# Kernel optimization log

Hardware: AMD Instinct MI355X
Metric: run time of the kernel (lower is better)

Reference implementation:

```python
import jax, jax.numpy as jnp
import numpy as np

B, D_MODEL, H, W = 4, 128, 128, 128
HEAD_DIM = 16
GROUP = D_MODEL // HEAD_DIM          # 8 deformable groups
D_INNER = D_MODEL                    # expand = 1
D_STATE = 1
DT_RANK = 8                          # ceil(d_model / 16)
D_CONV = 3
EPS = 1e-6


def setup_inputs() -> dict:
    key = jax.random.key(0)
    ks = jax.random.split(key, 10)
    f = jnp.float32
    # dt bias init as in DASSM.dt_init (dt in [1e-3, 1e-1], inverse-softplus)
    dt = jnp.exp(jax.random.uniform(ks[7], (D_INNER,), f)
                 * (np.log(0.1) - np.log(0.001)) + np.log(0.001))
    dt = jnp.clip(dt, 1e-4)
    dt_b = dt + jnp.log(-jnp.expm1(-dt))
    s = DT_RANK ** -0.5
    return dict(
        x=jax.random.normal(ks[0], (B, D_MODEL, H, W), f),
        in_proj_w=jax.random.normal(ks[1], (D_INNER, D_MODEL), f) * (D_MODEL ** -0.5),
        conv2d_w=jax.random.normal(ks[2], (D_INNER, 1, D_CONV, D_CONV), f) * 0.1,
        conv2d_b=jnp.zeros((D_INNER,), f),
        dw_w=jax.random.normal(ks[3], (D_INNER, 1, 3, 3), f) * 0.1,
        dw_b=jnp.zeros((D_INNER,), f),
        dw_ln_g=jnp.ones((D_INNER,), f),
        dw_ln_b=jnp.zeros((D_INNER,), f),
        off_w=jax.random.normal(ks[4], (GROUP * 2, D_INNER), f) * 0.01,
        off_b=jnp.zeros((GROUP * 2,), f),
        x_proj_w=jax.random.normal(ks[5], (DT_RANK + 2 * D_STATE, D_INNER), f) * (D_INNER ** -0.5),
        dt_w=jax.random.uniform(ks[6], (D_INNER, DT_RANK), f, -s, s),
        dt_b=dt_b,
        A_logs=jnp.tile(jnp.log(jnp.arange(1, D_STATE + 1, dtype=f))[None, :], (D_INNER, 1)),
        Ds=jnp.ones((D_INNER,), f),
        out_ln_g=jnp.ones((D_INNER,), f),
        out_ln_b=jnp.zeros((D_INNER,), f),
        out_proj_w=jax.random.normal(ks[8], (D_MODEL, D_INNER), f) * (D_INNER ** -0.5),
    )


def _layer_norm(x, g, b):
    m = x.mean(-1, keepdims=True)
    v = ((x - m) ** 2).mean(-1, keepdims=True)
    return (x - m) * jax.lax.rsqrt(v + EPS) * g + b


def _dwconv(x, w, b):
    # x: (B,C,H,W), w: (C,1,k,k) depthwise, 'SAME' == torch padding=(k-1)//2
    out = jax.lax.conv_general_dilated(
        x, w, (1, 1), 'SAME', feature_group_count=x.shape[1],
        dimension_numbers=('NCHW', 'OIHW', 'NCHW'))
    return out + b[None, :, None, None]


def _dcn_sample(img_last, offset):
    # DCNv3 with kernel_size=1, mask=1: sampling point = pixel center + offset.
    # img_last: (B,H,W,C); offset: (B,H,W,G*2) laid out (x,y) per group.
    b, h, w, c = img_last.shape
    gc = c // GROUP
    img = img_last.reshape(b, h, w, GROUP, gc)
    off = offset.reshape(b, h, w, GROUP, 2)
    px = jnp.arange(w, dtype=offset.dtype)[None, None, :, None] + off[..., 0]
    py = jnp.arange(h, dtype=offset.dtype)[None, :, None, None] + off[..., 1]
    y0 = jnp.floor(py)
    x0 = jnp.floor(px)
    wy = py - y0
    wx = px - x0
    bi = jnp.arange(b)[:, None, None, None]
    gi = jnp.arange(GROUP)[None, None, None, :]

    def tap(yi, xi, wgt):  # zero-padding bilinear tap (grid_sample, align_corners=False)
        valid = (yi >= 0) & (yi < h) & (xi >= 0) & (xi < w)
        yc = jnp.clip(yi, 0, h - 1).astype(jnp.int32)
        xc = jnp.clip(xi, 0, w - 1).astype(jnp.int32)
        v = img[bi, yc, xc, gi]  # (B,H,W,G,gc)
        return v * (wgt * valid)[..., None]

    out = (tap(y0, x0, (1 - wy) * (1 - wx)) + tap(y0, x0 + 1, (1 - wy) * wx)
           + tap(y0 + 1, x0, wy * (1 - wx)) + tap(y0 + 1, x0 + 1, wy * wx))
    return out.reshape(b, h, w, c)


def _selective_scan(xs, dts, A, Bs, Cs, Ds, dt_bias):
    # xs,dts: (B,D,L); A: (D,N); Bs,Cs: (B,N,L); delta_softplus=True
    delta = jax.nn.softplus(dts + dt_bias[None, :, None])
    dA = jnp.exp(jnp.einsum('bdl,dn->lbdn', delta, A))          # (L,B,D,N)
    dBx = jnp.einsum('bdl,bnl,bdl->lbdn', delta, Bs, xs)          # (L,B,D,N)
    C_t = jnp.transpose(Cs, (2, 0, 1))                            # (L,B,N)

    def step(hc, inputs):
        dA_t, dBx_t, c = inputs
        hc = dA_t * hc + dBx_t
        return hc, jnp.einsum('bdn,bn->bd', hc, c)

    h0 = jnp.zeros(dA.shape[1:], xs.dtype)
    _, ys = jax.lax.scan(step, h0, (dA, dBx, C_t))                # ys: (L,B,D)
    y = jnp.transpose(ys, (1, 2, 0))                              # (B,D,L)
    return y + Ds[None, :, None] * xs


def reference(x, in_proj_w, conv2d_w, conv2d_b, dw_w, dw_b, dw_ln_g, dw_ln_b,
              off_w, off_b, x_proj_w, dt_w, dt_b, A_logs, Ds,
              out_ln_g, out_ln_b, out_proj_w):
    # in_proj (1x1 conv, no bias) then depthwise conv + SiLU
    xin = jnp.einsum('bchw,oc->bohw', x, in_proj_w)
    xc = jax.nn.silu(_dwconv(xin, conv2d_w, conv2d_b))
    # Dynamic_Adaptive_Scan: dwconv -> LN(channels_last) -> GELU -> offsets -> DCNv3(k=1)
    x1 = _dwconv(xc, dw_w, dw_b)
    x1 = jax.nn.gelu(_layer_norm(jnp.transpose(x1, (0, 2, 3, 1)), dw_ln_g, dw_ln_b),
                     approximate=False)
    offset = x1 @ off_w.T + off_b                                  # (B,H,W,G*2)
    xd = _dcn_sample(jnp.transpose(xc, (0, 2, 3, 1)), offset)      # (B,H,W,C)
    xd = jnp.transpose(xd, (0, 3, 1, 2))                           # (B,C,H,W)
    # SSM (Mamba selective scan over L = H*W)
    Bn, C, Hh, Ww = xd.shape
    L = Hh * Ww
    xs = xd.reshape(Bn, C, L)
    x_dbl = jnp.einsum('rc,bcl->brl', x_proj_w, xs)
    dts, Bs, Cs = jnp.split(x_dbl, [DT_RANK, DT_RANK + D_STATE], axis=1)
    dts = jnp.einsum('dr,brl->bdl', dt_w, dts)
    A = -jnp.exp(A_logs)
    y = _selective_scan(xs, dts, A, Bs, Cs, Ds, dt_b).reshape(Bn, C, Hh, Ww)
    # out LayerNorm (over channels) + out_proj (1x1, no bias)
    y = jnp.transpose(_layer_norm(jnp.transpose(y, (0, 2, 3, 1)), out_ln_g, out_ln_b),
                      (0, 3, 1, 2))
    return jnp.einsum('bchw,oc->bohw', y, out_proj_w)
```

## Files before the change

kernel.cpp:

```cpp
#include <hip/hip_runtime.h>
#include <hip/hip_bf16.h>

typedef unsigned short u16;
typedef unsigned int u32;
typedef __bf16 bf16x8 __attribute__((ext_vector_type(8)));
typedef float f32x4 __attribute__((ext_vector_type(4)));

__device__ __forceinline__ float bfu(u16 u) { return __uint_as_float(((u32)u) << 16); }
__device__ __forceinline__ u16 fbf(float f) {
  __hip_bfloat16 h = __float2bfloat16(f);
  return *reinterpret_cast<u16*>(&h);
}
__device__ __forceinline__ float softplusf(float z) {
  float t = __expf(z);
  return (z > 20.f) ? z : __logf(1.f + t);
}
__device__ __forceinline__ float lo16(u32 p) { return __uint_as_float(p << 16); }
__device__ __forceinline__ float hi16(u32 p) { return __uint_as_float(p & 0xffff0000u); }
__device__ __forceinline__ bf16x8 ld_bf8(const u16* p) {
  union { uint4 u; bf16x8 v; } c;
  c.u = *(const uint4*)p;
  return c.v;
}

__global__ __launch_bounds__(256) void k_inproj(const float* __restrict__ X,
                                                const float* __restrict__ W,
                                                u16* __restrict__ out) {
  __shared__ __align__(16) u16 Ws[128 * 136];
  __shared__ __align__(16) u16 Xs[64 * 136];
  int tid = threadIdx.x;
  int b = blockIdx.x >> 8;
  int l0 = (blockIdx.x & 255) << 6;
  for (int i = 0; i < 16; ++i) {
    int idx = (i << 8) + tid;
    int o = idx >> 5, c4 = (idx & 31) << 2;
    float4 w4 = *(const float4*)&W[(o << 7) + c4];
    ushort4 s;
    s.x = fbf(w4.x); s.y = fbf(w4.y); s.z = fbf(w4.z); s.w = fbf(w4.w);
    *(ushort4*)&Ws[o * 136 + c4] = s;
  }
  for (int i = 0; i < 8; ++i) {
    int idx = (i << 8) + tid;
    int c = idx >> 4, lq = (idx & 15) << 2;
    float4 x4 = *(const float4*)&X[(((long)(b << 7) + c) << 14) + l0 + lq];
    Xs[(lq + 0) * 136 + c] = fbf(x4.x);
    Xs[(lq + 1) * 136 + c] = fbf(x4.y);
    Xs[(lq + 2) * 136 + c] = fbf(x4.z);
    Xs[(lq + 3) * 136 + c] = fbf(x4.w);
  }
  __syncthreads();
  int w = tid >> 6, lane = tid & 63;
  int mrow = lane & 15, quad = lane >> 4;
  f32x4 acc[2][4];
#pragma unroll
  for (int ot = 0; ot < 2; ++ot)
#pragma unroll
    for (int lt = 0; lt < 4; ++lt) acc[ot][lt] = (f32x4){0.f, 0.f, 0.f, 0.f};
#pragma unroll
  for (int kb = 0; kb < 4; ++kb) {
    int c0 = (kb << 5) + (quad << 3);
    bf16x8 af[2], bfr[4];
#pragma unroll
    for (int ot = 0; ot < 2; ++ot)
      af[ot] = ld_bf8(&Ws[((w << 5) + (ot << 4) + mrow) * 136 + c0]);
#pragma unroll
    for (int lt = 0; lt < 4; ++lt)
      bfr[lt] = ld_bf8(&Xs[((lt << 4) + mrow) * 136 + c0]);
#pragma unroll
    for (int ot = 0; ot < 2; ++ot)
#pragma unroll
      for (int lt = 0; lt < 4; ++lt)
        acc[ot][lt] = __builtin_amdgcn_mfma_f32_16x16x32_bf16(af[ot], bfr[lt], acc[ot][lt], 0, 0, 0);
  }
#pragma unroll
  for (int ot = 0; ot < 2; ++ot)
#pragma unroll
    for (int lt = 0; lt < 4; ++lt) {
      int l = l0 + (lt << 4) + mrow;
      int o = (w << 5) + (ot << 4) + (quad << 2);
      ushort4 s;
      s.x = fbf(acc[ot][lt][0]); s.y = fbf(acc[ot][lt][1]);
      s.z = fbf(acc[ot][lt][2]); s.w = fbf(acc[ot][lt][3]);
      *(ushort4*)&out[(((long)(b << 14) + l) << 7) + o] = s;
    }
}

__global__ __launch_bounds__(256) void k_dwconv(const u16* __restrict__ in,
                                                const float* __restrict__ w9,
                                                const float* __restrict__ bias,
                                                u16* __restrict__ out, int act) {
  __shared__ float wsT[9][128];
  __shared__ float bs[128];
  int tid = threadIdx.x;
  for (int i = 0; i < 5; ++i) {
    int lin = (i << 8) + tid;
    if (lin < 1152) { int c = lin / 9, k = lin - 9 * c; wsT[k][c] = w9[lin]; }
  }
  if (tid < 128) bs[tid] = bias[tid];
  __syncthreads();
  int blk = blockIdx.x;
  int b = blk >> 10;
  int s = blk & 1023;
  int h = s >> 3;
  int w = ((s & 7) << 4) + (tid >> 4);
  int c0 = (tid & 15) << 3;
  const u16* bbase = in + ((long)b << 21);
  float acc[8];
  {
    float4 b0 = *(const float4*)&bs[c0];
    float4 b1 = *(const float4*)&bs[c0 + 4];
    acc[0] = b0.x; acc[1] = b0.y; acc[2] = b0.z; acc[3] = b0.w;
    acc[4] = b1.x; acc[5] = b1.y; acc[6] = b1.z; acc[7] = b1.w;
  }
#pragma unroll
  for (int ky = -1; ky <= 1; ++ky) {
    int y = h + ky;
    if ((unsigned)y >= 128u) continue;
#pragma unroll
    for (int kx = -1; kx <= 1; ++kx) {
      int x = w + kx;
      if ((unsigned)x >= 128u) continue;
      int k = (ky + 1) * 3 + (kx + 1);
      uint4 v = *(const uint4*)(bbase + ((((y << 7) + x)) << 7) + c0);
      float4 w0 = *(const float4*)&wsT[k][c0];
      float4 w1 = *(const float4*)&wsT[k][c0 + 4];
      u32 vv[4] = {v.x, v.y, v.z, v.w};
      float wf[8] = {w0.x, w0.y, w0.z, w0.w, w1.x, w1.y, w1.z, w1.w};
#pragma unroll
      for (int cc = 0; cc < 8; ++cc) {
        float xv = (cc & 1) ? hi16(vv[cc >> 1]) : lo16(vv[cc >> 1]);
        acc[cc] = fmaf(wf[cc], xv, acc[cc]);
      }
    }
  }
  if (act) {
#pragma unroll
    for (int cc = 0; cc < 8; ++cc) acc[cc] = acc[cc] / (1.f + __expf(-acc[cc]));
  }
  ushort4 s0, s1;
  s0.x = fbf(acc[0]); s0.y = fbf(acc[1]); s0.z = fbf(acc[2]); s0.w = fbf(acc[3]);
  s1.x = fbf(acc[4]); s1.y = fbf(acc[5]); s1.z = fbf(acc[6]); s1.w = fbf(acc[7]);
  u16* po = out + ((long)b << 21) + ((((h << 7) + w)) << 7) + c0;
  *(ushort4*)po = s0;
  *(ushort4*)(po + 4) = s1;
}

__global__ __launch_bounds__(256) void k_offset(const u16* __restrict__ x1,
                                                const float* __restrict__ g,
                                                const float* __restrict__ bt,
                                                const float* __restrict__ offw,
                                                const float* __restrict__ offb,
                                                float* __restrict__ offs) {
  __shared__ float Wo[16 * 128];
  __shared__ float gs[128], bsh[128];
  int tid = threadIdx.x;
  if (tid < 128) { gs[tid] = g[tid]; bsh[tid] = bt[tid]; }
  for (int i = 0; i < 8; ++i) { int idx = (i << 8) + tid; Wo[idx] = offw[idx]; }
  __syncthreads();
  int pg = (blockIdx.x << 8) + tid;
  int b = pg >> 14, l = pg & 16383;
  const uint4* px = (const uint4*)(x1 + ((long)pg << 7));
  float s = 0.f, ss = 0.f;
  for (int i = 0; i < 16; ++i) {
    uint4 v = px[i];
    u32 vv[4] = {v.x, v.y, v.z, v.w};
#pragma unroll
    for (int cc = 0; cc < 8; ++cc) {
      float xv = (cc & 1) ? hi16(vv[cc >> 1]) : lo16(vv[cc >> 1]);
      s += xv; ss = fmaf(xv, xv, ss);
    }
  }
  float mean = s * (1.f / 128.f);
  float var = ss * (1.f / 128.f) - mean * mean;
  float rstd = rsqrtf(var + 1e-6f);
  float acc[16];
#pragma unroll
  for (int j = 0; j < 16; ++j) acc[j] = offb[j];
  for (int i = 0; i < 16; ++i) {
    uint4 v = px[i];
    u32 vv[4] = {v.x, v.y, v.z, v.w};
#pragma unroll
    for (int cc = 0; cc < 8; ++cc) {
      int c = (i << 3) + cc;
      float xv = (cc & 1) ? hi16(vv[cc >> 1]) : lo16(vv[cc >> 1]);
      float xn = fmaf((xv - mean) * rstd, gs[c], bsh[c]);
      float ge = 0.5f * xn * (1.f + erff(xn * 0.70710678118f));
#pragma unroll
      for (int j = 0; j < 16; ++j) acc[j] = fmaf(Wo[j * 128 + c], ge, acc[j]);
    }
  }
  float2* po = (float2*)offs;
#pragma unroll
  for (int gg = 0; gg < 8; ++gg)
    po[(((long)((b << 3) + gg)) << 14) + l] = make_float2(acc[2 * gg], acc[2 * gg + 1]);
}

__global__ __launch_bounds__(256) void k_dcn(const u16* __restrict__ xc,
                                             const float* __restrict__ offs,
                                             const float* __restrict__ xpw,
                                             const float* __restrict__ dtw,
                                             u16* __restrict__ xs,
                                             u16* __restrict__ dts,
                                             float* __restrict__ Bsb,
                                             float* __restrict__ Csb) {
  __shared__ float xds[32 * 129];
  __shared__ float xdbl[32 * 13];
  __shared__ float xpws[1280];
  __shared__ float dtws[1024];
  int tid = threadIdx.x;
  for (int i = 0; i < 5; ++i) { int idx = (i << 8) + tid; if (idx < 1280) xpws[idx] = xpw[idx]; }
  for (int i = 0; i < 4; ++i) { int idx = (i << 8) + tid; dtws[idx] = dtw[idx]; }
  int blk = blockIdx.x;
  int b = blk >> 9;
  int l0 = (blk & 511) << 5;
  int p = tid & 31, gg = tid >> 5;
  int l = l0 + p, hh = l >> 7, ww = l & 127;
  float2 off = ((const float2*)offs)[(((long)((b << 3) + gg)) << 14) + l];
  float px = (float)ww + off.x, py = (float)hh + off.y;
  float x0f = floorf(px), y0f = floorf(py);
  float wx = px - x0f, wy = py - y0f;
  int ix = (int)x0f, iy = (int)y0f;
  float acc[16];
#pragma unroll
  for (int ch = 0; ch < 16; ++ch) acc[ch] = 0.f;
  const u16* bbase = xc + ((long)b << 21) + (gg << 4);
  int xi[4] = {ix, ix + 1, ix, ix + 1};
  int yi[4] = {iy, iy, iy + 1, iy + 1};
  float wt4[4] = {(1.f - wy) * (1.f - wx), (1.f - wy) * wx, wy * (1.f - wx), wy * wx};
#pragma unroll
  for (int t = 0; t < 4; ++t) {
    if (wt4[t] != 0.f && (unsigned)yi[t] < 128u && (unsigned)xi[t] < 128u) {
      const u16* pp = bbase + ((((yi[t] << 7) + xi[t])) << 7);
      uint4 v0 = *(const uint4*)pp;
      uint4 v1 = *(const uint4*)(pp + 8);
      float wv = wt4[t];
      u32 vv[8] = {v0.x, v0.y, v0.z, v0.w, v1.x, v1.y, v1.z, v1.w};
#pragma unroll
      for (int ch = 0; ch < 16; ++ch) {
        float xv = (ch & 1) ? hi16(vv[ch >> 1]) : lo16(vv[ch >> 1]);
        acc[ch] = fmaf(wv, xv, acc[ch]);
      }
    }
  }
#pragma unroll
  for (int ch = 0; ch < 16; ++ch) xds[p * 129 + (gg << 4) + ch] = acc[ch];
  __syncthreads();
  for (int it = 0; it < 4; ++it) {
    int task = (it << 8) + tid;
    int cc = task >> 3, t = task & 7;
    ushort4 s;
    s.x = fbf(xds[(4 * t + 0) * 129 + cc]);
    s.y = fbf(xds[(4 * t + 1) * 129 + cc]);
    s.z = fbf(xds[(4 * t + 2) * 129 + cc]);
    s.w = fbf(xds[(4 * t + 3) * 129 + cc]);
    *(ushort4*)&xs[(((long)(b << 7) + cc) << 14) + l0 + (t << 2)] = s;
  }
  for (int task = tid; task < 320; task += 256) {
    int p2 = task / 10, r = task - p2 * 10;
    const float* wr = xpws + (r << 7);
    const float* xr = xds + p2 * 129;
    float sacc = 0.f;
#pragma unroll 8
    for (int cc = 0; cc < 128; ++cc) sacc = fmaf(wr[cc], xr[cc], sacc);
    xdbl[p2 * 13 + r] = sacc;
  }
  __syncthreads();
  for (int it = 0; it < 4; ++it) {
    int task = (it << 8) + tid;
    int dd = task >> 3, t = task & 7;
    const float* wd = dtws + (dd << 3);
    u16 sv[4];
#pragma unroll
    for (int j = 0; j < 4; ++j) {
      const float* xb = xdbl + (4 * t + j) * 13;
      float sacc = 0.f;
#pragma unroll
      for (int r = 0; r < 8; ++r) sacc = fmaf(wd[r], xb[r], sacc);
      sv[j] = fbf(sacc);
    }
    ushort4 s; s.x = sv[0]; s.y = sv[1]; s.z = sv[2]; s.w = sv[3];
    *(ushort4*)&dts[(((long)(b << 7) + dd) << 14) + l0 + (t << 2)] = s;
  }
  if (tid < 32) {
    Bsb[((long)b << 14) + l0 + tid] = xdbl[tid * 13 + 8];
    Csb[((long)b << 14) + l0 + tid] = xdbl[tid * 13 + 9];
  }
}

__global__ __launch_bounds__(1024) void k_scan(u16* __restrict__ xy,
                                               const u16* __restrict__ dts16,
                                               const float* __restrict__ Bsb,
                                               const float* __restrict__ Csb,
                                               const float* __restrict__ A_logs,
                                               const float* __restrict__ Dsv,
                                               const float* __restrict__ dtbv) {
  __shared__ float swp[16], swe[16];
  int bd = blockIdx.x;
  int b = bd >> 7, d = bd & 127;
  float Ad = -__expf(A_logs[d]);
  float dtb = dtbv[d];
  float Dd = Dsv[d];
  int t = threadIdx.x;
  int lane = t & 63, wid = t >> 6;
  long base = ((long)bd << 14) + (t << 4);
  long bb = ((long)b << 14) + (t << 4);
  const uint4* pz4 = (const uint4*)(dts16 + base);
  const uint4* px4 = (const uint4*)(xy + base);
  const float4* pB = (const float4*)(Bsb + bb);
  const float4* pC = (const float4*)(Csb + bb);
  uint4 zA = pz4[0], zB = pz4[1];
  uint4 xA = px4[0], xB = px4[1];
  u32 zw[8] = {zA.x, zA.y, zA.z, zA.w, zB.x, zB.y, zB.z, zB.w};
  u32 xw[8] = {xA.x, xA.y, xA.z, xA.w, xB.x, xB.y, xB.z, xB.w};
  float E = 0.f, P = 1.f;
#pragma unroll
  for (int q = 0; q < 4; ++q) {
    float4 B4 = pB[q];
    float Bq[4] = {B4.x, B4.y, B4.z, B4.w};
#pragma unroll
    for (int j = 0; j < 4; ++j) {
      int k = (q << 2) + j;
      float z = (k & 1) ? hi16(zw[k >> 1]) : lo16(zw[k >> 1]);
      float xv = (k & 1) ? hi16(xw[k >> 1]) : lo16(xw[k >> 1]);
      float delta = softplusf(z + dtb);
      float a = __expf(delta * Ad);
      E = fmaf(a, E, delta * Bq[j] * xv);
      P *= a;
    }
  }
#pragma unroll
  for (int off = 1; off < 64; off <<= 1) {
    float Pp = __shfl_up(P, off);
    float Ep = __shfl_up(E, off);
    if (lane >= off) { E = fmaf(P, Ep, E); P *= Pp; }
  }
  if (lane == 63) { swp[wid] = P; swe[wid] = E; }
  __syncthreads();
  if (t < 16) {
    float p2 = swp[t], e2 = swe[t];
#pragma unroll
    for (int off = 1; off < 16; off <<= 1) {
      float pp = __shfl_up(p2, off);
      float ee = __shfl_up(e2, off);
      if (t >= off) { e2 = fmaf(p2, ee, e2); p2 *= pp; }
    }
    swp[t] = p2; swe[t] = e2;
  }
  __syncthreads();
  float hw = (wid == 0) ? 0.f : swe[wid - 1];
  float Pex = __shfl_up(P, 1);
  float Eex = __shfl_up(E, 1);
  if (lane == 0) { Pex = 1.f; Eex = 0.f; }
  float h = fmaf(Pex, hw, Eex);
  u32 ypk[8];
#pragma unroll
  for (int q = 0; q < 4; ++q) {
    float4 B4 = pB[q];
    float4 C4 = pC[q];
    float Bq[4] = {B4.x, B4.y, B4.z, B4.w};
    float Cq[4] = {C4.x, C4.y, C4.z, C4.w};
#pragma unroll
    for (int j = 0; j < 4; ++j) {
      int k = (q << 2) + j;
      float z = (k & 1) ? hi16(zw[k >> 1]) : lo16(zw[k >> 1]);
      float xv = (k & 1) ? hi16(xw[k >> 1]) : lo16(xw[k >> 1]);
      float delta = softplusf(z + dtb);
      float a = __expf(delta * Ad);
      h = fmaf(a, h, delta * Bq[j] * xv);
      u16 yb = fbf(fmaf(Dd, xv, h * Cq[j]));
      if ((k & 1) == 0) ypk[k >> 1] = yb; else ypk[k >> 1] |= (u32)yb << 16;
    }
  }
  uint4* py = (uint4*)(xy + base);
  py[0] = make_uint4(ypk[0], ypk[1], ypk[2], ypk[3]);
  py[1] = make_uint4(ypk[4], ypk[5], ypk[6], ypk[7]);
}

__global__ void k_sums(const float* __restrict__ W2, const float* __restrict__ g,
                       const float* __restrict__ bln, float* __restrict__ s12) {
  int o = threadIdx.x;
  float s1 = 0.f, s2 = 0.f;
  for (int c = 0; c < 128; ++c) {
    float w = W2[(o << 7) + c];
    s1 = fmaf(w, bln[c], s1);
    s2 = fmaf(w, g[c], s2);
  }
  s12[o] = s1;
  s12[128 + o] = s2;
}

__global__ __launch_bounds__(256) void k_outproj(const u16* __restrict__ y,
                                                 const float* __restrict__ W2,
                                                 const float* __restrict__ g,
                                                 const float* __restrict__ s12,
                                                 float* __restrict__ out) {
  __shared__ __align__(16) u16 Ws[128 * 136];
  __shared__ __align__(16) u16 Ys[64 * 136];
  __shared__ float ps[4][64], pss[4][64];
  __shared__ float mean_s[64], rstd_s[64];
  int tid = threadIdx.x;
  int b = blockIdx.x >> 8;
  int l0 = (blockIdx.x & 255) << 6;
  for (int i = 0; i < 16; ++i) {
    int idx = (i << 8) + tid;
    int o = idx >> 5, c4 = (idx & 31) << 2;
    float4 w4 = *(const float4*)&W2[(o << 7) + c4];
    ushort4 s;
    s.x = fbf(w4.x * g[c4]);     s.y = fbf(w4.y * g[c4 + 1]);
    s.z = fbf(w4.z * g[c4 + 2]); s.w = fbf(w4.w * g[c4 + 3]);
    *(ushort4*)&Ws[o * 136 + c4] = s;
  }
  for (int i = 0; i < 4; ++i) {
    int idx = (i << 8) + tid;
    int c = idx >> 3, lq = (idx & 7) << 3;
    uint4 v = *(const uint4*)&y[(((long)(b << 7) + c) << 14) + l0 + lq];
    u32 vv[4] = {v.x, v.y, v.z, v.w};
#pragma unroll
    for (int r = 0; r < 8; ++r)
      Ys[(lq + r) * 136 + c] = (u16)((r & 1) ? (vv[r >> 1] >> 16) : (vv[r >> 1] & 0xffffu));
  }
  __syncthreads();
  {
    int l = tid & 63, q = tid >> 6;
    const u16* row = &Ys[l * 136 + (q << 5)];
    float s = 0.f, ss = 0.f;
#pragma unroll 8
    for (int c = 0; c < 32; ++c) { float v = bfu(row[c]); s += v; ss = fmaf(v, v, ss); }
    ps[q][l] = s; pss[q][l] = ss;
  }
  __syncthreads();
  if (tid < 64) {
    float s = ps[0][tid] + ps[1][tid] + ps[2][tid] + ps[3][tid];
    float ss = pss[0][tid] + pss[1][tid] + pss[2][tid] + pss[3][tid];
    float m = s * (1.f / 128.f);
    mean_s[tid] = m;
    rstd_s[tid] = rsqrtf(ss * (1.f / 128.f) - m * m + 1e-6f);
  }
  __syncthreads();
  int w = tid >> 6, lane = tid & 63;
  int mrow = lane & 15, quad = lane >> 4;
  f32x4 acc[2][4];
#pragma unroll
  for (int ot = 0; ot < 2; ++ot)
#pragma unroll
    for (int lt = 0; lt < 4; ++lt) acc[ot][lt] = (f32x4){0.f, 0.f, 0.f, 0.f};
#pragma unroll
  for (int kb = 0; kb < 4; ++kb) {
    int c0 = (kb << 5) + (quad << 3);
    bf16x8 af[2], bfr[4];
#pragma unroll
    for (int ot = 0; ot < 2; ++ot)
      af[ot] = ld_bf8(&Ws[((w << 5) + (ot << 4) + mrow) * 136 + c0]);
#pragma unroll
    for (int lt = 0; lt < 4; ++lt)
      bfr[lt] = ld_bf8(&Ys[((lt << 4) + mrow) * 136 + c0]);
#pragma unroll
    for (int ot = 0; ot < 2; ++ot)
#pragma unroll
      for (int lt = 0; lt < 4; ++lt)
        acc[ot][lt] = __builtin_amdgcn_mfma_f32_16x16x32_bf16(af[ot], bfr[lt], acc[ot][lt], 0, 0, 0);
  }
  float s1r[2][4], s2r[2][4];
#pragma unroll
  for (int ot = 0; ot < 2; ++ot)
#pragma unroll
    for (int r = 0; r < 4; ++r) {
      int o = (w << 5) + (ot << 4) + (quad << 2) + r;
      s1r[ot][r] = s12[o];
      s2r[ot][r] = s12[128 + o];
    }
#pragma unroll
  for (int ot = 0; ot < 2; ++ot)
#pragma unroll
    for (int lt = 0; lt < 4; ++lt) {
      int lcol = (lt << 4) + mrow;
      float mv = mean_s[lcol], rv = rstd_s[lcol];
      int obase = (w << 5) + (ot << 4) + (quad << 2);
#pragma unroll
      for (int r = 0; r < 4; ++r) {
        float v = fmaf(rv, acc[ot][lt][r] - mv * s2r[ot][r], s1r[ot][r]);
        out[(((long)(b << 7) + obase + r) << 14) + l0 + lcol] = v;
      }
    }
}

extern "C" void kernel_launch(void* const* d_in, const int* in_sizes, int n_in,
                              void* d_out, int out_size, void* d_ws, size_t ws_size,
                              hipStream_t stream) {
  const float* x         = (const float*)d_in[0];
  const float* in_proj_w = (const float*)d_in[1];
  const float* conv2d_w  = (const float*)d_in[2];
  const float* conv2d_b  = (const float*)d_in[3];
  const float* dw_w      = (const float*)d_in[4];
  const float* dw_b      = (const float*)d_in[5];
  const float* dw_ln_g   = (const float*)d_in[6];
  const float* dw_ln_b   = (const float*)d_in[7];
  const float* off_w     = (const float*)d_in[8];
  const float* off_b     = (const float*)d_in[9];
  const float* x_proj_w  = (const float*)d_in[10];
  const float* dt_w      = (const float*)d_in[11];
  const float* dt_b      = (const float*)d_in[12];
  const float* A_logs    = (const float*)d_in[13];
  const float* Ds        = (const float*)d_in[14];
  const float* out_ln_g  = (const float*)d_in[15];
  const float* out_ln_b  = (const float*)d_in[16];
  const float* out_proj_w= (const float*)d_in[17];
  float* out = (float*)d_out;

  u16* A  = (u16*)d_ws;
  u16* Bx = A + 8388608;
  u16* Dd = Bx + 8388608;
  float* offs  = (float*)(Dd + 8388608);
  float* Bsb   = offs + 1048576;
  float* Csb   = Bsb + 65536;
  float* s12   = Csb + 65536;

  hipLaunchKernelGGL(k_inproj, dim3(1024), dim3(256), 0, stream, x, in_proj_w, A);
  hipLaunchKernelGGL(k_dwconv, dim3(4096), dim3(256), 0, stream, A, conv2d_w, conv2d_b, Bx, 1);
  hipLaunchKernelGGL(k_dwconv, dim3(4096), dim3(256), 0, stream, Bx, dw_w, dw_b, A, 0);
  hipLaunchKernelGGL(k_offset, dim3(256), dim3(256), 0, stream, A, dw_ln_g, dw_ln_b, off_w, off_b, offs);
  hipLaunchKernelGGL(k_dcn, dim3(2048), dim3(256), 0, stream, Bx, offs, x_proj_w, dt_w, A, Dd, Bsb, Csb);
  hipLaunchKernelGGL(k_scan, dim3(512), dim3(1024), 0, stream, A, Dd, Bsb, Csb, A_logs, Ds, dt_b);
  hipLaunchKernelGGL(k_sums, dim3(1), dim3(128), 0, stream, out_proj_w, out_ln_g, out_ln_b, s12);
  hipLaunchKernelGGL(k_outproj, dim3(1024), dim3(256), 0, stream, A, out_proj_w, out_ln_g, s12, out);
}
```

Before: 246.7 us.

## Rewrite offset projection with MFMA and widen DCN tiles to 64 pixels

After: 235.7 us. -4.5%, faster.

```diff
diff --git a/kernel.cpp b/kernel.cpp
--- a/kernel.cpp
+++ b/kernel.cpp
@@ -151,51 +151,78 @@
                                                 const float* __restrict__ offw,
                                                 const float* __restrict__ offb,
                                                 float* __restrict__ offs) {
-  __shared__ float Wo[16 * 128];
+  __shared__ __align__(16) u16 Ge[64 * 136];
+  __shared__ __align__(16) u16 Wos[16 * 136];
+  __shared__ float ps[4][64], pss[4][64];
+  __shared__ float mean_s[64], rstd_s[64];
   __shared__ float gs[128], bsh[128];
   int tid = threadIdx.x;
+  int pg0 = blockIdx.x << 6;
+  int b = pg0 >> 14;
   if (tid < 128) { gs[tid] = g[tid]; bsh[tid] = bt[tid]; }
-  for (int i = 0; i < 8; ++i) { int idx = (i << 8) + tid; Wo[idx] = offw[idx]; }
-  __syncthreads();
-  int pg = (blockIdx.x << 8) + tid;
-  int b = pg >> 14, l = pg & 16383;
-  const uint4* px = (const uint4*)(x1 + ((long)pg << 7));
-  float s = 0.f, ss = 0.f;
-  for (int i = 0; i < 16; ++i) {
-    uint4 v = px[i];
-    u32 vv[4] = {v.x, v.y, v.z, v.w};
-#pragma unroll
-    for (int cc = 0; cc < 8; ++cc) {
-      float xv = (cc & 1) ? hi16(vv[cc >> 1]) : lo16(vv[cc >> 1]);
-      s += xv; ss = fmaf(xv, xv, ss);
-    }
-  }
-  float mean = s * (1.f / 128.f);
-  float var = ss * (1.f / 128.f) - mean * mean;
-  float rstd = rsqrtf(var + 1e-6f);
-  float acc[16];
-#pragma unroll
-  for (int j = 0; j < 16; ++j) acc[j] = offb[j];
-  for (int i = 0; i < 16; ++i) {
-    uint4 v = px[i];
-    u32 vv[4] = {v.x, v.y, v.z, v.w};
-#pragma unroll
-    for (int cc = 0; cc < 8; ++cc) {
-      int c = (i << 3) + cc;
-      float xv = (cc & 1) ? hi16(vv[cc >> 1]) : lo16(vv[cc >> 1]);
-      float xn = fmaf((xv - mean) * rstd, gs[c], bsh[c]);
-      float ge = 0.5f * xn * (1.f + erff(xn * 0.70710678118f));
-#pragma unroll
-      for (int j = 0; j < 16; ++j) acc[j] = fmaf(Wo[j * 128 + c], ge, acc[j]);
-    }
-  }
+  for (int i = 0; i < 8; ++i) {
+    int idx = (i << 8) + tid;
+    int o = idx >> 7, c = idx & 127;
+    Wos[o * 136 + c] = fbf(offw[idx]);
+  }
+  int l = tid >> 2, cq = (tid & 3) << 5;
+  {
+    const u16* px = x1 + (((long)(pg0 + l)) << 7) + cq;
+    float s = 0.f, ss = 0.f;
+#pragma unroll
+    for (int i2 = 0; i2 < 4; ++i2) {
+      uint4 v = *(const uint4*)(px + (i2 << 3));
+      *(uint4*)&Ge[l * 136 + cq + (i2 << 3)] = v;
+      u32 vv[4] = {v.x, v.y, v.z, v.w};
+#pragma unroll
+      for (int cc = 0; cc < 8; ++cc) {
+        float xv = (cc & 1) ? hi16(vv[cc >> 1]) : lo16(vv[cc >> 1]);
+        s += xv; ss = fmaf(xv, xv, ss);
+      }
+    }
+    ps[tid & 3][l] = s; pss[tid & 3][l] = ss;
+  }
+  __syncthreads();
+  if (tid < 64) {
+    float s = ps[0][tid] + ps[1][tid] + ps[2][tid] + ps[3][tid];
+    float ss = pss[0][tid] + pss[1][tid] + pss[2][tid] + pss[3][tid];
+    float m = s * (1.f / 128.f);
+    mean_s[tid] = m;
+    rstd_s[tid] = rsqrtf(ss * (1.f / 128.f) - m * m + 1e-6f);
+  }
+  __syncthreads();
+  {
+    float m = mean_s[l], r = rstd_s[l];
+    u16* row = &Ge[l * 136 + cq];
+#pragma unroll 8
+    for (int cc = 0; cc < 32; ++cc) {
+      int c = cq + cc;
+      float v = bfu(row[cc]);
+      float xn = fmaf((v - m) * r, gs[c], bsh[c]);
+      row[cc] = fbf(0.5f * xn * (1.f + erff(xn * 0.70710678118f)));
+    }
+  }
+  __syncthreads();
+  int w = tid >> 6, lane = tid & 63;
+  int mrow = lane & 15, quad = lane >> 4;
+  f32x4 acc0 = (f32x4){0.f, 0.f, 0.f, 0.f};
+#pragma unroll
+  for (int kb = 0; kb < 4; ++kb) {
+    int c0 = (kb << 5) + (quad << 3);
+    bf16x8 af = ld_bf8(&Wos[mrow * 136 + c0]);
+    bf16x8 bfr = ld_bf8(&Ge[((w << 4) + mrow) * 136 + c0]);
+    acc0 = __builtin_amdgcn_mfma_f32_16x16x32_bf16(af, bfr, acc0, 0, 0, 0);
+  }
+  int lg = (pg0 & 16383) + (w << 4) + mrow;
   float2* po = (float2*)offs;
-#pragma unroll
-  for (int gg = 0; gg < 8; ++gg)
-    po[(((long)((b << 3) + gg)) << 14) + l] = make_float2(acc[2 * gg], acc[2 * gg + 1]);
-}
-
-__global__ __launch_bounds__(256) void k_dcn(const u16* __restrict__ xc,
+  int o0 = quad << 2;
+  po[(((long)((b << 3) + (quad << 1))) << 14) + lg] =
+      make_float2(acc0[0] + offb[o0], acc0[1] + offb[o0 + 1]);
+  po[(((long)((b << 3) + (quad << 1) + 1)) << 14) + lg] =
+      make_float2(acc0[2] + offb[o0 + 2], acc0[3] + offb[o0 + 3]);
+}
+
+__global__ __launch_bounds__(512) void k_dcn(const u16* __restrict__ xc,
                                              const float* __restrict__ offs,
                                              const float* __restrict__ xpw,
                                              const float* __restrict__ dtw,
@@ -203,17 +230,17 @@
                                              u16* __restrict__ dts,
                                              float* __restrict__ Bsb,
                                              float* __restrict__ Csb) {
-  __shared__ float xds[32 * 129];
-  __shared__ float xdbl[32 * 13];
+  __shared__ float xds[64 * 129];
+  __shared__ float xdbl[64 * 13];
   __shared__ float xpws[1280];
   __shared__ float dtws[1024];
   int tid = threadIdx.x;
-  for (int i = 0; i < 5; ++i) { int idx = (i << 8) + tid; if (idx < 1280) xpws[idx] = xpw[idx]; }
-  for (int i = 0; i < 4; ++i) { int idx = (i << 8) + tid; dtws[idx] = dtw[idx]; }
+  for (int i = 0; i < 3; ++i) { int idx = (i << 9) + tid; if (idx < 1280) xpws[idx] = xpw[idx]; }
+  for (int i = 0; i < 2; ++i) { int idx = (i << 9) + tid; dtws[idx] = dtw[idx]; }
   int blk = blockIdx.x;
-  int b = blk >> 9;
-  int l0 = (blk & 511) << 5;
-  int p = tid & 31, gg = tid >> 5;
+  int b = blk >> 8;
+  int l0 = (blk & 255) << 6;
+  int p = tid & 63, gg = tid >> 6;
   int l = l0 + p, hh = l >> 7, ww = l & 127;
   float2 off = ((const float2*)offs)[(((long)((b << 3) + gg)) << 14) + l];
   float px = (float)ww + off.x, py = (float)hh + off.y;
@@ -245,17 +272,21 @@
 #pragma unroll
   for (int ch = 0; ch < 16; ++ch) xds[p * 129 + (gg << 4) + ch] = acc[ch];
   __syncthreads();
-  for (int it = 0; it < 4; ++it) {
-    int task = (it << 8) + tid;
+#pragma unroll
+  for (int it = 0; it < 2; ++it) {
+    int task = (it << 9) + tid;
     int cc = task >> 3, t = task & 7;
-    ushort4 s;
-    s.x = fbf(xds[(4 * t + 0) * 129 + cc]);
-    s.y = fbf(xds[(4 * t + 1) * 129 + cc]);
-    s.z = fbf(xds[(4 * t + 2) * 129 + cc]);
-    s.w = fbf(xds[(4 * t + 3) * 129 + cc]);
-    *(ushort4*)&xs[(((long)(b << 7) + cc) << 14) + l0 + (t << 2)] = s;
-  }
-  for (int task = tid; task < 320; task += 256) {
+    u32 pk[4];
+#pragma unroll
+    for (int jj = 0; jj < 4; ++jj) {
+      u16 a0 = fbf(xds[((t << 3) + 2 * jj + 0) * 129 + cc]);
+      u16 a1 = fbf(xds[((t << 3) + 2 * jj + 1) * 129 + cc]);
+      pk[jj] = (u32)a0 | ((u32)a1 << 16);
+    }
+    *(uint4*)&xs[(((long)(b << 7) + cc) << 14) + l0 + (t << 3)] =
+        make_uint4(pk[0], pk[1], pk[2], pk[3]);
+  }
+  for (int task = tid; task < 640; task += 512) {
     int p2 = task / 10, r = task - p2 * 10;
     const float* wr = xpws + (r << 7);
     const float* xr = xds + p2 * 129;
@@ -265,23 +296,29 @@
     xdbl[p2 * 13 + r] = sacc;
   }
   __syncthreads();
-  for (int it = 0; it < 4; ++it) {
-    int task = (it << 8) + tid;
+#pragma unroll
+  for (int it = 0; it < 2; ++it) {
+    int task = (it << 9) + tid;
     int dd = task >> 3, t = task & 7;
     const float* wd = dtws + (dd << 3);
-    u16 sv[4];
-#pragma unroll
-    for (int j = 0; j < 4; ++j) {
-      const float* xb = xdbl + (4 * t + j) * 13;
-      float sacc = 0.f;
-#pragma unroll
-      for (int r = 0; r < 8; ++r) sacc = fmaf(wd[r], xb[r], sacc);
-      sv[j] = fbf(sacc);
-    }
-    ushort4 s; s.x = sv[0]; s.y = sv[1]; s.z = sv[2]; s.w = sv[3];
-    *(ushort4*)&dts[(((long)(b << 7) + dd) << 14) + l0 + (t << 2)] = s;
-  }
-  if (tid < 32) {
+    u32 pk[4];
+#pragma unroll
+    for (int jj = 0; jj < 4; ++jj) {
+      u16 h2[2];
+#pragma unroll
+      for (int hh2 = 0; hh2 < 2; ++hh2) {
+        const float* xb = xdbl + ((t << 3) + 2 * jj + hh2) * 13;
+        float sacc = 0.f;
+#pragma unroll
+        for (int r = 0; r < 8; ++r) sacc = fmaf(wd[r], xb[r], sacc);
+        h2[hh2] = fbf(sacc);
+      }
+      pk[jj] = (u32)h2[0] | ((u32)h2[1] << 16);
+    }
+    *(uint4*)&dts[(((long)(b << 7) + dd) << 14) + l0 + (t << 3)] =
+        make_uint4(pk[0], pk[1], pk[2], pk[3]);
+  }
+  if (tid < 64) {
     Bsb[((long)b << 14) + l0 + tid] = xdbl[tid * 13 + 8];
     Csb[((long)b << 14) + l0 + tid] = xdbl[tid * 13 + 9];
   }
@@ -518,8 +555,8 @@
   hipLaunchKernelGGL(k_inproj, dim3(1024), dim3(256), 0, stream, x, in_proj_w, A);
   hipLaunchKernelGGL(k_dwconv, dim3(4096), dim3(256), 0, stream, A, conv2d_w, conv2d_b, Bx, 1);
   hipLaunchKernelGGL(k_dwconv, dim3(4096), dim3(256), 0, stream, Bx, dw_w, dw_b, A, 0);
-  hipLaunchKernelGGL(k_offset, dim3(256), dim3(256), 0, stream, A, dw_ln_g, dw_ln_b, off_w, off_b, offs);
-  hipLaunchKernelGGL(k_dcn, dim3(2048), dim3(256), 0, stream, Bx, offs, x_proj_w, dt_w, A, Dd, Bsb, Csb);
+  hipLaunchKernelGGL(k_offset, dim3(1024), dim3(256), 0, stream, A, dw_ln_g, dw_ln_b, off_w, off_b, offs);
+  hipLaunchKernelGGL(k_dcn, dim3(1024), dim3(512), 0, stream, Bx, offs, x_proj_w, dt_w, A, Dd, Bsb, Csb);
   hipLaunchKernelGGL(k_scan, dim3(512), dim3(1024), 0, stream, A, Dd, Bsb, Csb, A_logs, Ds, dt_b);
   hipLaunchKernelGGL(k_sums, dim3(1), dim3(128), 0, stream, out_proj_w, out_ln_g, out_ln_b, s12);
   hipLaunchKernelGGL(k_outproj, dim3(1024), dim3(256), 0, stream, A, out_proj_w, out_ln_g, s12, out);
```
